# Performance work log

Measured on AMD Instinct MI355X. Metric: run time of the kernel, lower is better.

Reference implementation:

```python
import jax, jax.numpy as jnp
import numpy as np

TOKENS = 8192
HIDDEN = 4096
EPS = 1e-6
FP8_MAX = 448.0  # max finite value of float8_e4m3fn


def setup_inputs() -> dict:
    key = jax.random.key(0)
    k1, k2, k3 = jax.random.split(key, 3)
    x = jax.random.normal(k1, (TOKENS, HIDDEN), jnp.float32)
    # RMSNorm gains near 1
    norm_w = 1.0 + 0.1 * jax.random.normal(k2, (4, HIDDEN), jnp.float32)
    Ws = 0.02 * jax.random.normal(k3, (3, HIDDEN, HIDDEN), jnp.float32)
    # static per-tensor weight scales (amax / fp8_max)
    w_scales = jnp.max(jnp.abs(Ws), axis=(1, 2)) / FP8_MAX
    return {"x": x, "norm_w": norm_w, "Ws": Ws, "w_scales": w_scales}


def _rmsnorm(x, w):
    var = jnp.mean(x * x, axis=-1, keepdims=True)
    return x * jax.lax.rsqrt(var + EPS) * w


def _quant_dequant_fp8(v, s):
    # quantize to e4m3 with scale s, then dequantize (emulated fp8 GEMM inputs)
    q = (v / s).astype(jnp.float8_e4m3fn)
    return q.astype(jnp.float32) * s


def _fp8_linear(y, W, w_scale):
    # dynamic per-token activation scale
    a_scale = jnp.maximum(jnp.max(jnp.abs(y), axis=-1, keepdims=True) / FP8_MAX, 1e-12)
    yq = _quant_dequant_fp8(y, a_scale)           # [T, H]
    Wq = _quant_dequant_fp8(W, w_scale)           # [H, H]
    return yq @ Wq.T                              # torch.nn.Linear convention


def reference(x, norm_w, Ws, w_scales):
    x = jax.nn.relu(x)
    resid = x
    y = _rmsnorm(x, norm_w[0])                    # plain RMSNorm
    for i in range(3):
        h = _fp8_linear(y, Ws[i], w_scales[i])    # FP8 GEMM
        resid = h + resid                         # fused add + RMSNorm
        y = _rmsnorm(resid, norm_w[i + 1])
    return y
```

## Files before the change

### kernel.cpp

```cpp
#include <hip/hip_runtime.h>
#include <stdint.h>

#define TOKENS 8192
#define HIDDEN 4096
constexpr float EPS = 1e-6f;
constexpr float FP8_MAX = 448.0f;

using f32x4  = __attribute__((ext_vector_type(4))) float;
using f32x16 = __attribute__((ext_vector_type(16))) float;
using i32x4  = __attribute__((ext_vector_type(4))) int;
using i32x8  = __attribute__((ext_vector_type(8))) int;

typedef __attribute__((address_space(3))) uint32_t lds_u32_t;
typedef const __attribute__((address_space(1))) uint32_t glb_u32_t;

__device__ inline uint32_t pack_fp8x4(float a, float b, float c, float d) {
    int w = 0;
    w = __builtin_amdgcn_cvt_pk_fp8_f32(a, b, w, false);
    w = __builtin_amdgcn_cvt_pk_fp8_f32(c, d, w, true);
    return (uint32_t)w;
}

__device__ inline float block_sum(float v, float* sh, int tid) {
#pragma unroll
    for (int o = 32; o > 0; o >>= 1) v += __shfl_xor(v, o, 64);
    if ((tid & 63) == 0) sh[tid >> 6] = v;
    __syncthreads();
    return sh[0] + sh[1] + sh[2] + sh[3];
}
__device__ inline float block_max(float v, float* sh, int tid) {
#pragma unroll
    for (int o = 32; o > 0; o >>= 1) v = fmaxf(v, __shfl_xor(v, o, 64));
    if ((tid & 63) == 0) sh[tid >> 6] = v;
    __syncthreads();
    return fmaxf(fmaxf(sh[0], sh[1]), fmaxf(sh[2], sh[3]));
}

__launch_bounds__(256)
__global__ void quant_weights(const float* __restrict__ Ws,
                              const float* __restrict__ w_scales,
                              uint8_t* __restrict__ Wq) {
    size_t idx = ((size_t)blockIdx.x * 256 + threadIdx.x) * 8;
    int tensor = (int)(idx / ((size_t)HIDDEN * HIDDEN));
    float inv = 1.0f / w_scales[tensor];
    const float4* src = (const float4*)(Ws + idx);
    float4 v0 = src[0], v1 = src[1];
    uint2 out;
    out.x = pack_fp8x4(v0.x * inv, v0.y * inv, v0.z * inv, v0.w * inv);
    out.y = pack_fp8x4(v1.x * inv, v1.y * inv, v1.z * inv, v1.w * inv);
    *(uint2*)(Wq + idx) = out;
}

__launch_bounds__(256)
__global__ void relu_rms_quant(const float* __restrict__ x,
                               const float* __restrict__ nw,
                               float* __restrict__ resid,
                               uint8_t* __restrict__ yq,
                               float* __restrict__ ascale) {
    __shared__ float sh1[4], sh2[4];
    const int row = blockIdx.x, tid = threadIdx.x;
    const float* xr = x + (size_t)row * HIDDEN;
    float* rr = resid + (size_t)row * HIDDEN;

    float4 v[4];
    float ss = 0.f;
#pragma unroll
    for (int c = 0; c < 4; ++c) {
        float4 t = *(const float4*)(xr + c * 1024 + tid * 4);
        t.x = fmaxf(t.x, 0.f); t.y = fmaxf(t.y, 0.f);
        t.z = fmaxf(t.z, 0.f); t.w = fmaxf(t.w, 0.f);
        v[c] = t;
        ss += t.x * t.x + t.y * t.y + t.z * t.z + t.w * t.w;
        *(float4*)(rr + c * 1024 + tid * 4) = t;
    }
    ss = block_sum(ss, sh1, tid);
    float rstd = 1.0f / sqrtf(ss * (1.0f / HIDDEN) + EPS);

    float4 y[4];
    float amax = 0.f;
#pragma unroll
    for (int c = 0; c < 4; ++c) {
        float4 w = *(const float4*)(nw + c * 1024 + tid * 4);
        y[c].x = v[c].x * rstd * w.x; amax = fmaxf(amax, fabsf(y[c].x));
        y[c].y = v[c].y * rstd * w.y; amax = fmaxf(amax, fabsf(y[c].y));
        y[c].z = v[c].z * rstd * w.z; amax = fmaxf(amax, fabsf(y[c].z));
        y[c].w = v[c].w * rstd * w.w; amax = fmaxf(amax, fabsf(y[c].w));
    }
    amax = block_max(amax, sh2, tid);
    float s = fmaxf(amax / FP8_MAX, 1e-12f);
    if (tid == 0) ascale[row] = s;
    float inv = 1.0f / s;
#pragma unroll
    for (int c = 0; c < 4; ++c) {
        uint32_t p = pack_fp8x4(y[c].x * inv, y[c].y * inv, y[c].z * inv, y[c].w * inv);
        *(uint32_t*)(yq + (size_t)row * HIDDEN + c * 1024 + tid * 4) = p;
    }
}

__launch_bounds__(256)
__global__ void rms_quant(const float* __restrict__ resid,
                          const float* __restrict__ nw,
                          uint8_t* __restrict__ yq,
                          float* __restrict__ ascale) {
    __shared__ float sh1[4], sh2[4];
    const int row = blockIdx.x, tid = threadIdx.x;
    const float* rr = resid + (size_t)row * HIDDEN;

    float4 v[4];
    float ss = 0.f;
#pragma unroll
    for (int c = 0; c < 4; ++c) {
        float4 t = *(const float4*)(rr + c * 1024 + tid * 4);
        v[c] = t;
        ss += t.x * t.x + t.y * t.y + t.z * t.z + t.w * t.w;
    }
    ss = block_sum(ss, sh1, tid);
    float rstd = 1.0f / sqrtf(ss * (1.0f / HIDDEN) + EPS);

    float4 y[4];
    float amax = 0.f;
#pragma unroll
    for (int c = 0; c < 4; ++c) {
        float4 w = *(const float4*)(nw + c * 1024 + tid * 4);
        y[c].x = v[c].x * rstd * w.x; amax = fmaxf(amax, fabsf(y[c].x));
        y[c].y = v[c].y * rstd * w.y; amax = fmaxf(amax, fabsf(y[c].y));
        y[c].z = v[c].z * rstd * w.z; amax = fmaxf(amax, fabsf(y[c].z));
        y[c].w = v[c].w * rstd * w.w; amax = fmaxf(amax, fabsf(y[c].w));
    }
    amax = block_max(amax, sh2, tid);
    float s = fmaxf(amax / FP8_MAX, 1e-12f);
    if (tid == 0) ascale[row] = s;
    float inv = 1.0f / s;
#pragma unroll
    for (int c = 0; c < 4; ++c) {
        uint32_t p = pack_fp8x4(y[c].x * inv, y[c].y * inv, y[c].z * inv, y[c].w * inv);
        *(uint32_t*)(yq + (size_t)row * HIDDEN + c * 1024 + tid * 4) = p;
    }
}

__launch_bounds__(256)
__global__ void rms_final(const float* __restrict__ resid,
                          const float* __restrict__ nw,
                          float* __restrict__ out) {
    __shared__ float sh1[4];
    const int row = blockIdx.x, tid = threadIdx.x;
    const float* rr = resid + (size_t)row * HIDDEN;

    float4 v[4];
    float ss = 0.f;
#pragma unroll
    for (int c = 0; c < 4; ++c) {
        float4 t = *(const float4*)(rr + c * 1024 + tid * 4);
        v[c] = t;
        ss += t.x * t.x + t.y * t.y + t.z * t.z + t.w * t.w;
    }
    ss = block_sum(ss, sh1, tid);
    float rstd = 1.0f / sqrtf(ss * (1.0f / HIDDEN) + EPS);

#pragma unroll
    for (int c = 0; c < 4; ++c) {
        float4 w = *(const float4*)(nw + c * 1024 + tid * 4);
        float4 o;
        o.x = v[c].x * rstd * w.x;
        o.y = v[c].y * rstd * w.y;
        o.z = v[c].z * rstd * w.z;
        o.w = v[c].w * rstd * w.w;
        *(float4*)(out + (size_t)row * HIDDEN + c * 1024 + tid * 4) = o;
    }
}

#define BM 256
#define BN 256
#define BK 64
#define NBUF 4

__launch_bounds__(512, 2)
__global__ void gemm_fp8(const uint8_t* __restrict__ Aq,
                         const uint8_t* __restrict__ Bq,
                         const float* __restrict__ ascale,
                         const float* __restrict__ wscale_p,
                         float* __restrict__ resid) {
    __shared__ __align__(16) uint8_t sA[NBUF][BM * BK];
    __shared__ __align__(16) uint8_t sB[NBUF][BN * BK];
    __shared__ float s_as[BM];

    const int tid = threadIdx.x;
    int bid = blockIdx.x;
    bid = (bid & 7) * 64 + (bid >> 3);
    const int nbn = HIDDEN / BN;
    const int bm = bid / nbn, bn = bid % nbn;
    const int brow = bm * BM, bcol = bn * BN;

    const int wave = tid >> 6, lane = tid & 63;
    const int wm = wave >> 2, wn = wave & 3;
    const int lr = lane & 31;
    const int lh = lane >> 5;

    f32x16 acc[4][2] = {};

    const uint8_t* aSrc = Aq + (size_t)brow * HIDDEN;
    const uint8_t* bSrc = Bq + (size_t)bcol * HIDDEN;

    const int r_st = tid >> 2;
    const int g_st = tid & 3;
    const int gsrc = g_st ^ ((r_st >> 1) & 3);
    const size_t off0 = (size_t)r_st * HIDDEN + gsrc * 16;
    const size_t off1 = (size_t)(r_st + 128) * HIDDEN + gsrc * 16;
    const int ldsw = wave * 1024;

    int offA[4][2], offB[2][2];
#pragma unroll
    for (int mi = 0; mi < 4; ++mi) {
        int ra = wm * 128 + mi * 32 + lr;
        int sw = (ra >> 1) & 3;
        offA[mi][0] = ra * 64 + ((2 * lh + 0) ^ sw) * 16;
        offA[mi][1] = ra * 64 + ((2 * lh + 1) ^ sw) * 16;
    }
#pragma unroll
    for (int ni = 0; ni < 2; ++ni) {
        int rb = wn * 64 + ni * 32 + lr;
        int sw = (rb >> 1) & 3;
        offB[ni][0] = rb * 64 + ((2 * lh + 0) ^ sw) * 16;
        offB[ni][1] = rb * 64 + ((2 * lh + 1) ^ sw) * 16;
    }

    const int UNIT = 0x7F7F7F7F;

    auto stage = [&](int buf, int kt) {
        const int k0 = kt * BK;
        __builtin_amdgcn_global_load_lds((glb_u32_t*)(aSrc + off0 + k0),
                                         (lds_u32_t*)&sA[buf][ldsw], 16, 0, 0);
        __builtin_amdgcn_global_load_lds((glb_u32_t*)(aSrc + off1 + k0),
                                         (lds_u32_t*)&sA[buf][8192 + ldsw], 16, 0, 0);
        __builtin_amdgcn_global_load_lds((glb_u32_t*)(bSrc + off0 + k0),
                                         (lds_u32_t*)&sB[buf][ldsw], 16, 0, 0);
        __builtin_amdgcn_global_load_lds((glb_u32_t*)(bSrc + off1 + k0),
                                         (lds_u32_t*)&sB[buf][8192 + ldsw], 16, 0, 0);
    };
    auto compute = [&](int buf) {
        i32x8 a[4], b[2];
#pragma unroll
        for (int mi = 0; mi < 4; ++mi) {
            i32x4 lo = *(const i32x4*)&sA[buf][offA[mi][0]];
            i32x4 hi = *(const i32x4*)&sA[buf][offA[mi][1]];
            a[mi] = __builtin_shufflevector(lo, hi, 0, 1, 2, 3, 4, 5, 6, 7);
        }
#pragma unroll
        for (int ni = 0; ni < 2; ++ni) {
            i32x4 lo = *(const i32x4*)&sB[buf][offB[ni][0]];
            i32x4 hi = *(const i32x4*)&sB[buf][offB[ni][1]];
            b[ni] = __builtin_shufflevector(lo, hi, 0, 1, 2, 3, 4, 5, 6, 7);
        }
        __builtin_amdgcn_s_setprio(1);
#pragma unroll
        for (int mi = 0; mi < 4; ++mi)
#pragma unroll
            for (int ni = 0; ni < 2; ++ni)
                acc[mi][ni] = __builtin_amdgcn_mfma_scale_f32_32x32x64_f8f6f4(
                    a[mi], b[ni], acc[mi][ni], 0, 0, 0, UNIT, 0, UNIT);
        __builtin_amdgcn_s_setprio(0);
    };

    const int NT = HIDDEN / BK;
    stage(0, 0);
    stage(1, 1);
    for (int t = 0; t < NT; ++t) {
        if (t + 2 < NT) {
            stage((t + 2) & 3, t + 2);
            asm volatile("s_waitcnt vmcnt(8)" ::: "memory");
        } else if (t + 1 < NT) {
            asm volatile("s_waitcnt vmcnt(4)" ::: "memory");
        } else {
            asm volatile("s_waitcnt vmcnt(0)" ::: "memory");
        }
        __builtin_amdgcn_s_barrier();
        compute(t & 3);
    }

    if (tid < BM) s_as[tid] = ascale[brow + tid];
    __syncthreads();

    const float wsc = *wscale_p;
#pragma unroll
    for (int mi = 0; mi < 4; ++mi)
#pragma unroll
        for (int ni = 0; ni < 2; ++ni) {
            const int col = bcol + wn * 64 + ni * 32 + lr;
#pragma unroll
            for (int i = 0; i < 16; ++i) {
                const int rl = (i & 3) + 8 * (i >> 2) + 4 * lh;
                const int row_local = wm * 128 + mi * 32 + rl;
                const float alpha = s_as[row_local] * wsc;
                const size_t o = (size_t)(brow + row_local) * HIDDEN + col;
                resid[o] += acc[mi][ni][i] * alpha;
            }
        }
}

extern "C" void kernel_launch(void* const* d_in, const int* in_sizes, int n_in,
                              void* d_out, int out_size, void* d_ws, size_t ws_size,
                              hipStream_t stream) {
    const float* x   = (const float*)d_in[0];
    const float* nw  = (const float*)d_in[1];
    const float* Ws  = (const float*)d_in[2];
    const float* wsc = (const float*)d_in[3];
    float* out = (float*)d_out;

    uint8_t* ws = (uint8_t*)d_ws;
    float*   resid  = (float*)ws;
    uint8_t* yq     = ws + (size_t)TOKENS * HIDDEN * 4;
    uint8_t* Wq     = yq + (size_t)TOKENS * HIDDEN;
    float*   ascale = (float*)(Wq + (size_t)3 * HIDDEN * HIDDEN);

    quant_weights<<<(3 * (size_t)HIDDEN * HIDDEN) / 2048, 256, 0, stream>>>(Ws, wsc, Wq);

    relu_rms_quant<<<TOKENS, 256, 0, stream>>>(x, nw, resid, yq, ascale);

    for (int i = 0; i < 3; ++i) {
        gemm_fp8<<<(TOKENS / BM) * (HIDDEN / BN), 512, 0, stream>>>(
            yq, Wq + (size_t)i * HIDDEN * HIDDEN, ascale, wsc + i, resid);
        if (i < 2)
            rms_quant<<<TOKENS, 256, 0, stream>>>(resid, nw + (size_t)(i + 1) * HIDDEN, yq, ascale);
        else
            rms_final<<<TOKENS, 256, 0, stream>>>(resid, nw + (size_t)3 * HIDDEN, out);
    }
}
```

Before: 691.0 us.

## Split FP8 GEMM main loop into two half-phases interleaving LDS reads, loads, MFMA

Restructures the FP8 GEMM K-loop into two phases per tile. Each phase reads half of the A fragments from LDS, issues half of the next-next tile's global-to-LDS loads (A in the first phase, B in the second), then runs four MFMAs under raised priority, with barriers between phases. The prefetch depth grows from two tiles to three across the four LDS buffers. The aim is to overlap LDS fragment reads and global loads with MFMA work and to lower peak register use. The epilogue also hoists the per-row alpha computation out of the column loop. In exchange it adds several extra workgroup barriers per iteration.

```diff
diff --git a/kernel.cpp b/kernel.cpp
--- a/kernel.cpp
+++ b/kernel.cpp
@@ -226,55 +226,78 @@
 
     const int UNIT = 0x7F7F7F7F;
 
-    auto stage = [&](int buf, int kt) {
+    auto stageA = [&](int buf, int kt) {
         const int k0 = kt * BK;
         __builtin_amdgcn_global_load_lds((glb_u32_t*)(aSrc + off0 + k0),
                                          (lds_u32_t*)&sA[buf][ldsw], 16, 0, 0);
         __builtin_amdgcn_global_load_lds((glb_u32_t*)(aSrc + off1 + k0),
                                          (lds_u32_t*)&sA[buf][8192 + ldsw], 16, 0, 0);
+    };
+    auto stageB = [&](int buf, int kt) {
+        const int k0 = kt * BK;
         __builtin_amdgcn_global_load_lds((glb_u32_t*)(bSrc + off0 + k0),
                                          (lds_u32_t*)&sB[buf][ldsw], 16, 0, 0);
         __builtin_amdgcn_global_load_lds((glb_u32_t*)(bSrc + off1 + k0),
                                          (lds_u32_t*)&sB[buf][8192 + ldsw], 16, 0, 0);
     };
-    auto compute = [&](int buf) {
-        i32x8 a[4], b[2];
-#pragma unroll
-        for (int mi = 0; mi < 4; ++mi) {
-            i32x4 lo = *(const i32x4*)&sA[buf][offA[mi][0]];
-            i32x4 hi = *(const i32x4*)&sA[buf][offA[mi][1]];
-            a[mi] = __builtin_shufflevector(lo, hi, 0, 1, 2, 3, 4, 5, 6, 7);
-        }
+    auto rdfrag = [&](const uint8_t* base, const int* off) -> i32x8 {
+        i32x4 lo = *(const i32x4*)&base[off[0]];
+        i32x4 hi = *(const i32x4*)&base[off[1]];
+        return __builtin_shufflevector(lo, hi, 0, 1, 2, 3, 4, 5, 6, 7);
+    };
+
+    const int NT = HIDDEN / BK;
+    stageA(0, 0); stageB(0, 0);
+    stageA(1, 1); stageB(1, 1);
+    stageA(2, 2); stageB(2, 2);
+    asm volatile("s_waitcnt vmcnt(8)" ::: "memory");
+    __builtin_amdgcn_s_barrier();
+
+    i32x8 b01[2];
+    for (int t = 0; t < NT; ++t) {
+        const int buf = t & 3;
+        i32x8 a0 = rdfrag(sA[buf], offA[0]);
+        i32x8 a1 = rdfrag(sA[buf], offA[1]);
+        b01[0] = rdfrag(sB[buf], offB[0]);
+        b01[1] = rdfrag(sB[buf], offB[1]);
+        if (t + 3 < NT) stageA((t + 3) & 3, t + 3);
+        __builtin_amdgcn_s_barrier();
+        asm volatile("s_waitcnt lgkmcnt(0)" ::: "memory");
+        __builtin_amdgcn_sched_barrier(0);
+        __builtin_amdgcn_s_setprio(1);
 #pragma unroll
         for (int ni = 0; ni < 2; ++ni) {
-            i32x4 lo = *(const i32x4*)&sB[buf][offB[ni][0]];
-            i32x4 hi = *(const i32x4*)&sB[buf][offB[ni][1]];
-            b[ni] = __builtin_shufflevector(lo, hi, 0, 1, 2, 3, 4, 5, 6, 7);
-        }
-        __builtin_amdgcn_s_setprio(1);
-#pragma unroll
-        for (int mi = 0; mi < 4; ++mi)
-#pragma unroll
-            for (int ni = 0; ni < 2; ++ni)
-                acc[mi][ni] = __builtin_amdgcn_mfma_scale_f32_32x32x64_f8f6f4(
-                    a[mi], b[ni], acc[mi][ni], 0, 0, 0, UNIT, 0, UNIT);
+            acc[0][ni] = __builtin_amdgcn_mfma_scale_f32_32x32x64_f8f6f4(
+                a0, b01[ni], acc[0][ni], 0, 0, 0, UNIT, 0, UNIT);
+            acc[1][ni] = __builtin_amdgcn_mfma_scale_f32_32x32x64_f8f6f4(
+                a1, b01[ni], acc[1][ni], 0, 0, 0, UNIT, 0, UNIT);
+        }
         __builtin_amdgcn_s_setprio(0);
-    };
-
-    const int NT = HIDDEN / BK;
-    stage(0, 0);
-    stage(1, 1);
-    for (int t = 0; t < NT; ++t) {
-        if (t + 2 < NT) {
-            stage((t + 2) & 3, t + 2);
+        __builtin_amdgcn_s_barrier();
+
+        i32x8 a2 = rdfrag(sA[buf], offA[2]);
+        i32x8 a3 = rdfrag(sA[buf], offA[3]);
+        if (t + 3 < NT) {
+            stageB((t + 3) & 3, t + 3);
             asm volatile("s_waitcnt vmcnt(8)" ::: "memory");
-        } else if (t + 1 < NT) {
+        } else if (t + 2 < NT) {
             asm volatile("s_waitcnt vmcnt(4)" ::: "memory");
         } else {
             asm volatile("s_waitcnt vmcnt(0)" ::: "memory");
         }
         __builtin_amdgcn_s_barrier();
-        compute(t & 3);
+        asm volatile("s_waitcnt lgkmcnt(0)" ::: "memory");
+        __builtin_amdgcn_sched_barrier(0);
+        __builtin_amdgcn_s_setprio(1);
+#pragma unroll
+        for (int ni = 0; ni < 2; ++ni) {
+            acc[2][ni] = __builtin_amdgcn_mfma_scale_f32_32x32x64_f8f6f4(
+                a2, b01[ni], acc[2][ni], 0, 0, 0, UNIT, 0, UNIT);
+            acc[3][ni] = __builtin_amdgcn_mfma_scale_f32_32x32x64_f8f6f4(
+                a3, b01[ni], acc[3][ni], 0, 0, 0, UNIT, 0, UNIT);
+        }
+        __builtin_amdgcn_s_setprio(0);
+        __builtin_amdgcn_s_barrier();
     }
 
     if (tid < BM) s_as[tid] = ascale[brow + tid];
@@ -282,7 +305,13 @@
 
     const float wsc = *wscale_p;
 #pragma unroll
-    for (int mi = 0; mi < 4; ++mi)
+    for (int mi = 0; mi < 4; ++mi) {
+        float alpha[16];
+#pragma unroll
+        for (int i = 0; i < 16; ++i) {
+            const int rl = (i & 3) + 8 * (i >> 2) + 4 * lh;
+            alpha[i] = s_as[wm * 128 + mi * 32 + rl] * wsc;
+        }
 #pragma unroll
         for (int ni = 0; ni < 2; ++ni) {
             const int col = bcol + wn * 64 + ni * 32 + lr;
@@ -290,11 +319,11 @@
             for (int i = 0; i < 16; ++i) {
                 const int rl = (i & 3) + 8 * (i >> 2) + 4 * lh;
                 const int row_local = wm * 128 + mi * 32 + rl;
-                const float alpha = s_as[row_local] * wsc;
                 const size_t o = (size_t)(brow + row_local) * HIDDEN + col;
-                resid[o] += acc[mi][ni][i] * alpha;
+                resid[o] += acc[mi][ni][i] * alpha[i];
             }
         }
+    }
 }
 
 extern "C" void kernel_launch(void* const* d_in, const int* in_sizes, int n_in,
```

Result: slower. 724.5 us (+4.8%).

## Double-buffer LDS fragment reads in registers to overlap with MFMA in FP8 GEMM

Applied to the files above, without the earlier changes.

Restructures the GEMM main loop so LDS fragments for the next k-tile are read into a second register set while MFMAs run on the current set, unrolled by two with ping-pong Frags. Prefetch depth goes from two to three tiles ahead across the 4 LDS buffers. The launch bound's min-blocks hint is dropped so the compiler can use more registers for the extra fragments. The activation-scale LDS fill moves to the kernel prologue, and per-row alphas are hoisted out of the epilogue loop. The cost is higher register pressure and possibly lower occupancy, and the new barrier/waitcnt sequencing makes buffer reuse more fragile.

```diff
diff --git a/kernel.cpp b/kernel.cpp
--- a/kernel.cpp
+++ b/kernel.cpp
@@ -174,7 +174,7 @@
 #define BK 64
 #define NBUF 4
 
-__launch_bounds__(512, 2)
+__launch_bounds__(512)
 __global__ void gemm_fp8(const uint8_t* __restrict__ Aq,
                          const uint8_t* __restrict__ Bq,
                          const float* __restrict__ ascale,
@@ -195,6 +195,8 @@
     const int wm = wave >> 2, wn = wave & 3;
     const int lr = lane & 31;
     const int lh = lane >> 5;
+
+    if (tid < BM) s_as[tid] = ascale[brow + tid];
 
     f32x16 acc[4][2] = {};
 
@@ -237,52 +239,76 @@
         __builtin_amdgcn_global_load_lds((glb_u32_t*)(bSrc + off1 + k0),
                                          (lds_u32_t*)&sB[buf][8192 + ldsw], 16, 0, 0);
     };
-    auto compute = [&](int buf) {
-        i32x8 a[4], b[2];
+
+    struct Frags { i32x8 a[4]; i32x8 b[2]; };
+    auto rdfrags = [&](int buf) -> Frags {
+        Frags f;
 #pragma unroll
         for (int mi = 0; mi < 4; ++mi) {
             i32x4 lo = *(const i32x4*)&sA[buf][offA[mi][0]];
             i32x4 hi = *(const i32x4*)&sA[buf][offA[mi][1]];
-            a[mi] = __builtin_shufflevector(lo, hi, 0, 1, 2, 3, 4, 5, 6, 7);
+            f.a[mi] = __builtin_shufflevector(lo, hi, 0, 1, 2, 3, 4, 5, 6, 7);
         }
 #pragma unroll
         for (int ni = 0; ni < 2; ++ni) {
             i32x4 lo = *(const i32x4*)&sB[buf][offB[ni][0]];
             i32x4 hi = *(const i32x4*)&sB[buf][offB[ni][1]];
-            b[ni] = __builtin_shufflevector(lo, hi, 0, 1, 2, 3, 4, 5, 6, 7);
-        }
+            f.b[ni] = __builtin_shufflevector(lo, hi, 0, 1, 2, 3, 4, 5, 6, 7);
+        }
+        return f;
+    };
+    auto mfma_all = [&](const Frags& f) {
         __builtin_amdgcn_s_setprio(1);
 #pragma unroll
         for (int mi = 0; mi < 4; ++mi)
 #pragma unroll
             for (int ni = 0; ni < 2; ++ni)
                 acc[mi][ni] = __builtin_amdgcn_mfma_scale_f32_32x32x64_f8f6f4(
-                    a[mi], b[ni], acc[mi][ni], 0, 0, 0, UNIT, 0, UNIT);
+                    f.a[mi], f.b[ni], acc[mi][ni], 0, 0, 0, UNIT, 0, UNIT);
         __builtin_amdgcn_s_setprio(0);
     };
+    auto wait_tiles = [&](int rem) {
+        if (rem >= 2)      asm volatile("s_waitcnt vmcnt(8)" ::: "memory");
+        else if (rem == 1) asm volatile("s_waitcnt vmcnt(4)" ::: "memory");
+        else               asm volatile("s_waitcnt vmcnt(0)" ::: "memory");
+    };
 
     const int NT = HIDDEN / BK;
-    stage(0, 0);
-    stage(1, 1);
-    for (int t = 0; t < NT; ++t) {
+    stage(0, 0); stage(1, 1); stage(2, 2);
+    asm volatile("s_waitcnt vmcnt(8)" ::: "memory");
+    __builtin_amdgcn_s_barrier();
+    __builtin_amdgcn_sched_barrier(0);
+    Frags fa = rdfrags(0);
+    Frags fb;
+
+#pragma unroll 1
+    for (int t = 0; t < NT; t += 2) {
+        if (t + 3 < NT) stage((t + 3) & 3, t + 3);
+        wait_tiles(((t + 3 < NT) ? t + 3 : NT - 1) - (t + 1));
+        __builtin_amdgcn_s_barrier();
+        __builtin_amdgcn_sched_barrier(0);
+        fb = rdfrags((t + 1) & 3);
+        mfma_all(fa);
+
+        if (t + 4 < NT) stage((t + 4) & 3, t + 4);
         if (t + 2 < NT) {
-            stage((t + 2) & 3, t + 2);
-            asm volatile("s_waitcnt vmcnt(8)" ::: "memory");
-        } else if (t + 1 < NT) {
-            asm volatile("s_waitcnt vmcnt(4)" ::: "memory");
-        } else {
-            asm volatile("s_waitcnt vmcnt(0)" ::: "memory");
-        }
-        __builtin_amdgcn_s_barrier();
-        compute(t & 3);
-    }
-
-    if (tid < BM) s_as[tid] = ascale[brow + tid];
-    __syncthreads();
+            wait_tiles(((t + 4 < NT) ? t + 4 : NT - 1) - (t + 2));
+            __builtin_amdgcn_s_barrier();
+            __builtin_amdgcn_sched_barrier(0);
+            fa = rdfrags((t + 2) & 3);
+        }
+        mfma_all(fb);
+    }
 
     const float wsc = *wscale_p;
 #pragma unroll
-    for (int mi = 0; mi < 4; ++mi)
+    for (int mi = 0; mi < 4; ++mi) {
+        float alpha[16];
+#pragma unroll
+        for (int i = 0; i < 16; ++i) {
+            const int rl = (i & 3) + 8 * (i >> 2) + 4 * lh;
+            alpha[i] = s_as[wm * 128 + mi * 32 + rl] * wsc;
+        }
 #pragma unroll
         for (int ni = 0; ni < 2; ++ni) {
             const int col = bcol + wn * 64 + ni * 32 + lr;
@@ -290,11 +316,11 @@
             for (int i = 0; i < 16; ++i) {
                 const int rl = (i & 3) + 8 * (i >> 2) + 4 * lh;
                 const int row_local = wm * 128 + mi * 32 + rl;
-                const float alpha = s_as[row_local] * wsc;
                 const size_t o = (size_t)(brow + row_local) * HIDDEN + col;
-                resid[o] += acc[mi][ni][i] * alpha;
+                resid[o] += acc[mi][ni][i] * alpha[i];
             }
         }
+    }
 }
 
 extern "C" void kernel_launch(void* const* d_in, const int* in_sizes, int n_in,
```

New measurement: 1.814 ms. 163% more time.

## Load GEMM A operand straight from global into registers, skipping LDS

Applied to the files above, without the earlier changes.

The FP8 GEMM now stages only B in LDS. Each wave reads its own A fragments directly from global memory into double-buffered registers, and the loop is unrolled by two to ping-pong the A registers. The intent is to halve LDS traffic and capacity and cut LDS reads for A. In exchange, the four waves sharing the same A rows load them redundantly from cache, register pressure rises, and the second half-iteration uses the B buffer with no barrier. The per-row activation scale is also loaded earlier and hoisted out of the epilogue loop.

```diff
diff --git a/kernel.cpp b/kernel.cpp
--- a/kernel.cpp
+++ b/kernel.cpp
@@ -180,7 +180,6 @@
                          const float* __restrict__ ascale,
                          const float* __restrict__ wscale_p,
                          float* __restrict__ resid) {
-    __shared__ __align__(16) uint8_t sA[NBUF][BM * BK];
     __shared__ __align__(16) uint8_t sB[NBUF][BN * BK];
     __shared__ float s_as[BM];
 
@@ -196,10 +195,17 @@
     const int lr = lane & 31;
     const int lh = lane >> 5;
 
+    if (tid < BM) s_as[tid] = ascale[brow + tid];
+
     f32x16 acc[4][2] = {};
 
     const uint8_t* aSrc = Aq + (size_t)brow * HIDDEN;
     const uint8_t* bSrc = Bq + (size_t)bcol * HIDDEN;
+
+    const uint8_t* aRow[4];
+#pragma unroll
+    for (int mi = 0; mi < 4; ++mi)
+        aRow[mi] = aSrc + (size_t)(wm * 128 + mi * 32 + lr) * HIDDEN + lh * 32;
 
     const int r_st = tid >> 2;
     const int g_st = tid & 3;
@@ -208,14 +214,7 @@
     const size_t off1 = (size_t)(r_st + 128) * HIDDEN + gsrc * 16;
     const int ldsw = wave * 1024;
 
-    int offA[4][2], offB[2][2];
-#pragma unroll
-    for (int mi = 0; mi < 4; ++mi) {
-        int ra = wm * 128 + mi * 32 + lr;
-        int sw = (ra >> 1) & 3;
-        offA[mi][0] = ra * 64 + ((2 * lh + 0) ^ sw) * 16;
-        offA[mi][1] = ra * 64 + ((2 * lh + 1) ^ sw) * 16;
-    }
+    int offB[2][2];
 #pragma unroll
     for (int ni = 0; ni < 2; ++ni) {
         int rb = wn * 64 + ni * 32 + lr;
@@ -226,63 +225,72 @@
 
     const int UNIT = 0x7F7F7F7F;
 
-    auto stage = [&](int buf, int kt) {
+    auto stageB = [&](int buf, int kt) {
         const int k0 = kt * BK;
-        __builtin_amdgcn_global_load_lds((glb_u32_t*)(aSrc + off0 + k0),
-                                         (lds_u32_t*)&sA[buf][ldsw], 16, 0, 0);
-        __builtin_amdgcn_global_load_lds((glb_u32_t*)(aSrc + off1 + k0),
-                                         (lds_u32_t*)&sA[buf][8192 + ldsw], 16, 0, 0);
         __builtin_amdgcn_global_load_lds((glb_u32_t*)(bSrc + off0 + k0),
                                          (lds_u32_t*)&sB[buf][ldsw], 16, 0, 0);
         __builtin_amdgcn_global_load_lds((glb_u32_t*)(bSrc + off1 + k0),
                                          (lds_u32_t*)&sB[buf][8192 + ldsw], 16, 0, 0);
     };
-    auto compute = [&](int buf) {
-        i32x8 a[4], b[2];
+    auto loadA = [&](i32x8 (&dst)[4], int kt) {
+        const int k0 = kt * BK;
 #pragma unroll
         for (int mi = 0; mi < 4; ++mi) {
-            i32x4 lo = *(const i32x4*)&sA[buf][offA[mi][0]];
-            i32x4 hi = *(const i32x4*)&sA[buf][offA[mi][1]];
-            a[mi] = __builtin_shufflevector(lo, hi, 0, 1, 2, 3, 4, 5, 6, 7);
+            i32x4 lo = *(const i32x4*)(aRow[mi] + k0);
+            i32x4 hi = *(const i32x4*)(aRow[mi] + k0 + 16);
+            dst[mi] = __builtin_shufflevector(lo, hi, 0, 1, 2, 3, 4, 5, 6, 7);
         }
-#pragma unroll
-        for (int ni = 0; ni < 2; ++ni) {
-            i32x4 lo = *(const i32x4*)&sB[buf][offB[ni][0]];
-            i32x4 hi = *(const i32x4*)&sB[buf][offB[ni][1]];
-            b[ni] = __builtin_shufflevector(lo, hi, 0, 1, 2, 3, 4, 5, 6, 7);
+    };
+    auto compute = [&](int buf, i32x8 (&A)[4]) {
+        i32x4 b0l = *(const i32x4*)&sB[buf][offB[0][0]];
+        i32x4 b0h = *(const i32x4*)&sB[buf][offB[0][1]];
+        i32x4 b1l = *(const i32x4*)&sB[buf][offB[1][0]];
+        i32x4 b1h = *(const i32x4*)&sB[buf][offB[1][1]];
+        i32x8 b0 = __builtin_shufflevector(b0l, b0h, 0, 1, 2, 3, 4, 5, 6, 7);
+        i32x8 b1 = __builtin_shufflevector(b1l, b1h, 0, 1, 2, 3, 4, 5, 6, 7);
+        __builtin_amdgcn_s_setprio(1);
+#pragma unroll
+        for (int mi = 0; mi < 4; ++mi) {
+            acc[mi][0] = __builtin_amdgcn_mfma_scale_f32_32x32x64_f8f6f4(
+                A[mi], b0, acc[mi][0], 0, 0, 0, UNIT, 0, UNIT);
+            acc[mi][1] = __builtin_amdgcn_mfma_scale_f32_32x32x64_f8f6f4(
+                A[mi], b1, acc[mi][1], 0, 0, 0, UNIT, 0, UNIT);
         }
-        __builtin_amdgcn_s_setprio(1);
-#pragma unroll
-        for (int mi = 0; mi < 4; ++mi)
-#pragma unroll
-            for (int ni = 0; ni < 2; ++ni)
-                acc[mi][ni] = __builtin_amdgcn_mfma_scale_f32_32x32x64_f8f6f4(
-                    a[mi], b[ni], acc[mi][ni], 0, 0, 0, UNIT, 0, UNIT);
         __builtin_amdgcn_s_setprio(0);
     };
 
     const int NT = HIDDEN / BK;
-    stage(0, 0);
-    stage(1, 1);
-    for (int t = 0; t < NT; ++t) {
-        if (t + 2 < NT) {
-            stage((t + 2) & 3, t + 2);
-            asm volatile("s_waitcnt vmcnt(8)" ::: "memory");
-        } else if (t + 1 < NT) {
-            asm volatile("s_waitcnt vmcnt(4)" ::: "memory");
-        } else {
-            asm volatile("s_waitcnt vmcnt(0)" ::: "memory");
+    i32x8 A0[4], A1[4];
+
+    stageB(0, 0); stageB(1, 1);
+    loadA(A0, 0);
+
+#pragma unroll 1
+    for (int t = 0; t < NT; t += 2) {
+        if (t + 2 < NT) stageB((t + 2) & 3, t + 2);
+        loadA(A1, t + 1);
+        if (t + 2 < NT) asm volatile("s_waitcnt vmcnt(10)" ::: "memory");
+        else            asm volatile("s_waitcnt vmcnt(8)"  ::: "memory");
+        __builtin_amdgcn_s_barrier();
+        compute(t & 3, A0);
+
+        if (t + 3 < NT) stageB((t + 3) & 3, t + 3);
+        if (t + 2 < NT) loadA(A0, t + 2);
+        if (t + 3 < NT)      asm volatile("s_waitcnt vmcnt(10)" ::: "memory");
+        else if (t + 2 < NT) asm volatile("s_waitcnt vmcnt(8)"  ::: "memory");
+        else                 asm volatile("s_waitcnt vmcnt(0)"  ::: "memory");
+        compute((t + 1) & 3, A1);
+    }
+
+    const float wsc = *wscale_p;
+#pragma unroll
+    for (int mi = 0; mi < 4; ++mi) {
+        float alpha[16];
+#pragma unroll
+        for (int i = 0; i < 16; ++i) {
+            const int rl = (i & 3) + 8 * (i >> 2) + 4 * lh;
+            alpha[i] = s_as[wm * 128 + mi * 32 + rl] * wsc;
         }
-        __builtin_amdgcn_s_barrier();
-        compute(t & 3);
-    }
-
-    if (tid < BM) s_as[tid] = ascale[brow + tid];
-    __syncthreads();
-
-    const float wsc = *wscale_p;
-#pragma unroll
-    for (int mi = 0; mi < 4; ++mi)
 #pragma unroll
         for (int ni = 0; ni < 2; ++ni) {
             const int col = bcol + wn * 64 + ni * 32 + lr;
@@ -290,11 +298,11 @@
             for (int i = 0; i < 16; ++i) {
                 const int rl = (i & 3) + 8 * (i >> 2) + 4 * lh;
                 const int row_local = wm * 128 + mi * 32 + rl;
-                const float alpha = s_as[row_local] * wsc;
                 const size_t o = (size_t)(brow + row_local) * HIDDEN + col;
-                resid[o] += acc[mi][ni][i] * alpha;
+                resid[o] += acc[mi][ni][i] * alpha[i];
             }
         }
+    }
 }
 
 extern "C" void kernel_launch(void* const* d_in, const int* in_sizes, int n_in,
```

Result: slower. 1.041 ms (+50.7%).
